# Optimization experiments

Hardware: AMD Instinct MI355X
Metric: run time of the kernel (lower is better)

The kernel has to match this reference:

```python
import jax, jax.numpy as jnp
import numpy as np

N_HEAD, D_FEAT, D_MODEL, D_ATTN = 4, 32, 32, 1
B, LQ, LK, H, W = 2, 24, 24, 16, 16
NEG_SLOPE = 0.1


def _lrelu(x):
    return jnp.where(x >= 0, x, NEG_SLOPE * x)


def setup_inputs() -> dict:
    key = jax.random.key(0)
    ks = jax.random.split(key, 12)
    s = 0.05
    inp = {
        "q": jax.random.normal(ks[0], (B, LQ, D_FEAT, H, W), jnp.float32),
        "k": jax.random.normal(ks[1], (B, LK, D_FEAT, H, W), jnp.float32),
        "v": jax.random.normal(ks[2], (B, LK, D_FEAT, H, W), jnp.float32),
        # 1x1 convs stored as (out_ch, in_ch) matrices
        "wq": jax.random.normal(ks[3], (N_HEAD * D_MODEL, D_FEAT), jnp.float32) * s,
        "bq": jax.random.normal(ks[4], (N_HEAD * D_MODEL,), jnp.float32) * s,
        "wk": jax.random.normal(ks[5], (N_HEAD * D_MODEL, D_FEAT), jnp.float32) * s,
        "bk": jax.random.normal(ks[6], (N_HEAD * D_MODEL,), jnp.float32) * s,
        "wv": jax.random.normal(ks[7], (N_HEAD * D_MODEL, D_FEAT), jnp.float32) * s,
        "bv": jax.random.normal(ks[8], (N_HEAD * D_MODEL,), jnp.float32) * s,
        # 5x5 attention conv (OIHW)
        "w_attn": jax.random.normal(ks[9], (D_ATTN, D_MODEL, 5, 5), jnp.float32) * s,
        "b_attn": jax.random.normal(ks[10], (D_ATTN,), jnp.float32) * s,
        # final Linear(n_head*d_model -> d_model), torch weight layout (out, in)
        "w_fc": jax.random.normal(ks[11], (D_MODEL, N_HEAD * D_MODEL), jnp.float32) * s,
    }
    return inp


def _proj_heads(x, w, b):
    # x: (b, l, c, h, w); 1x1 conv + leaky relu, split heads -> (b, n, l, d, h, w)
    y = _lrelu(jnp.einsum('blchw,oc->blohw', x, w) + b[None, None, :, None, None])
    bb, ll = x.shape[0], x.shape[1]
    return y.reshape(bb, ll, N_HEAD, D_MODEL, H, W).transpose(0, 2, 1, 3, 4, 5)


def reference(q, k, v, wq, bq, wk, bk, wv, bv, w_attn, b_attn, w_fc):
    qh = _proj_heads(q, wq, bq)  # (b,n,lq,d,h,w)
    kh = _proj_heads(k, wk, bk)  # (b,n,lk,d,h,w)
    vh = _proj_heads(v, wv, bv)  # (b,n,lk,d,h,w)

    # additive attention features: q_i + k_j for all (i,j) pairs
    qk = qh[:, :, :, None] + kh[:, :, None]  # (b,n,lq,lk,d,h,w)
    x = qk.reshape(-1, D_MODEL, H, W)
    logits = jax.lax.conv_general_dilated(
        x, w_attn, window_strides=(1, 1), padding=[(2, 2), (2, 2)],
        dimension_numbers=('NCHW', 'OIHW', 'NCHW')) + b_attn[None, :, None, None]
    attn = logits.reshape(B, N_HEAD, LQ, LK, D_ATTN, H, W)
    attn = jax.nn.softmax(attn, axis=3)  # softmax over keys

    # weighted sum over keys (d_attention==1 broadcasts over channels)
    res = jnp.einsum('bnqkhw,bnkchw->bnqchw', attn[:, :, :, :, 0], vh)

    # merge heads and apply final linear over channel dim (no bias), dropout=eval identity
    out = res.transpose(0, 2, 1, 3, 4, 5).reshape(B, LQ, N_HEAD * D_MODEL, H, W)
    out = jnp.einsum('blchw,oc->blohw', out, w_fc)  # (b,lq,d_model,h,w)
    return out, attn
```

## Files before the change

### kernel.cpp

```cpp
#include <hip/hip_runtime.h>
#include <math.h>

#define BB   2
#define LQ   24
#define LK   24
#define NH   4
#define DM   32
#define DF   32
#define HW   256
#define NEG  0.1f

#define PITCH 24
#define CHPAD (20 * PITCH)

__device__ __forceinline__ float lrelu(float x) { return x >= 0.f ? x : NEG * x; }

__global__ __launch_bounds__(256) void k_proj_conv(
    const float* __restrict__ kin, const float* __restrict__ vin,
    const float* __restrict__ wk, const float* __restrict__ bk,
    const float* __restrict__ wv, const float* __restrict__ bv,
    const float* __restrict__ wat,
    float* __restrict__ vh, float* __restrict__ ck)
{
    const int bx  = blockIdx.x;
    const int img = bx >> 2;
    const int cg  = bx & 3;
    const int b   = img / (NH * LK);
    const int n   = (img / LK) % NH;
    const int j   = img % LK;
    const int hw  = threadIdx.x;
    const int h   = hw >> 4, w = hw & 15;

    __shared__ float skh[8][CHPAD];

    for (int idx = hw; idx < 8 * CHPAD; idx += 256) ((float*)skh)[idx] = 0.f;

    const float* kb = kin + (size_t)((b * LK + j) * DF) * HW + hw;
    const float* vb = vin + (size_t)((b * LK + j) * DF) * HW + hw;

    float xr[DF];

    #pragma unroll
    for (int c = 0; c < DF; c++) xr[c] = vb[c * HW];
    #pragma unroll
    for (int d = 0; d < 8; d++) {
        const int o = n * DM + cg * 8 + d;
        const float* wr = wv + o * DF;
        float acc = bv[o];
        #pragma unroll
        for (int c = 0; c < DF; c++) acc += xr[c] * wr[c];
        vh[(size_t)img * (DM * HW) + (cg * 8 + d) * HW + hw] = lrelu(acc);
    }

    #pragma unroll
    for (int c = 0; c < DF; c++) xr[c] = kb[c * HW];
    __syncthreads();
    #pragma unroll
    for (int d = 0; d < 8; d++) {
        const int o = n * DM + cg * 8 + d;
        const float* wr = wk + o * DF;
        float acc = bk[o];
        #pragma unroll
        for (int c = 0; c < DF; c++) acc += xr[c] * wr[c];
        skh[d][(h + 2) * PITCH + (w + 2)] = lrelu(acc);
    }
    __syncthreads();

    float acc = 0.f;
    #pragma unroll
    for (int lc = 0; lc < 8; lc++) {
        const float* wc = wat + (cg * 8 + lc) * 25;
        #pragma unroll
        for (int ky = 0; ky < 5; ky++) {
            const float* row = &skh[lc][(h + ky) * PITCH + w];
            #pragma unroll
            for (int kx = 0; kx < 5; kx++)
                acc += row[kx] * wc[ky * 5 + kx];
        }
    }
    atomicAdd(&ck[img * HW + hw], acc);
}

__global__ __launch_bounds__(256) void k_softmax_res(
    const float* __restrict__ ck, const float* __restrict__ vh,
    float* __restrict__ res, float* __restrict__ attn_out)
{
    const int bn = blockIdx.x >> 5;
    const int u  = blockIdx.x & 31;
    const int hw = threadIdx.x;

    float e[LK];
    const float* cb = ck + bn * LK * HW + hw;
    float m = -1e30f;
    #pragma unroll
    for (int jj = 0; jj < LK; jj++) { e[jj] = cb[jj * HW]; m = fmaxf(m, e[jj]); }
    float s = 0.f;
    #pragma unroll
    for (int jj = 0; jj < LK; jj++) { e[jj] = __expf(e[jj] - m); s += e[jj]; }
    const float inv = 1.f / s;
    #pragma unroll
    for (int jj = 0; jj < LK; jj++) e[jj] *= inv;

    if (u < LQ) {
        float* ao = attn_out + (size_t)((bn * LQ + u) * LK) * HW + hw;
        #pragma unroll
        for (int jj = 0; jj < LK; jj++) ao[jj * HW] = e[jj];
    }

    const float* vp = vh + (size_t)(bn * LK) * (DM * HW) + u * HW + hw;
    float acc = 0.f;
    #pragma unroll
    for (int jj = 0; jj < LK; jj++) acc += e[jj] * vp[(size_t)jj * DM * HW];
    res[(bn * DM + u) * HW + hw] = acc;
}

__global__ __launch_bounds__(256) void k_fc(
    const float* __restrict__ res, const float* __restrict__ wfc,
    float* __restrict__ out)
{
    const int bx = blockIdx.x;
    const int b  = bx >> 7;
    const int o  = (bx >> 2) & 31;
    const int lg = bx & 3;
    const int hw = threadIdx.x;

    const float* rp = res + (size_t)b * (NH * DM) * HW + hw;
    const float* wr = wfc + o * (NH * DM);
    float acc = 0.f;
    #pragma unroll
    for (int nc = 0; nc < NH * DM; nc++) acc += wr[nc] * rp[nc * HW];

    #pragma unroll
    for (int l = lg * 6; l < lg * 6 + 6; l++)
        out[(size_t)((b * LQ + l) * DM + o) * HW + hw] = acc;
}

extern "C" void kernel_launch(void* const* d_in, const int* in_sizes, int n_in,
                              void* d_out, int out_size, void* d_ws, size_t ws_size,
                              hipStream_t stream)
{
    const float* k_in = (const float*)d_in[1];
    const float* v_in = (const float*)d_in[2];
    const float* wk   = (const float*)d_in[5];
    const float* bk   = (const float*)d_in[6];
    const float* wv   = (const float*)d_in[7];
    const float* bv   = (const float*)d_in[8];
    const float* wat  = (const float*)d_in[9];
    const float* wfc  = (const float*)d_in[11];

    float* out  = (float*)d_out;
    float* attn = out + (size_t)BB * LQ * DM * HW;

    float* vh  = (float*)d_ws;
    float* ck  = vh + (size_t)BB * NH * LK * DM * HW;
    float* res = ck + (size_t)BB * NH * LK * HW;

    hipMemsetAsync(ck, 0, (size_t)BB * NH * LK * HW * sizeof(float), stream);
    hipLaunchKernelGGL(k_proj_conv, dim3(BB * NH * LK * 4), dim3(256), 0, stream,
                       k_in, v_in, wk, bk, wv, bv, wat, vh, ck);
    hipLaunchKernelGGL(k_softmax_res, dim3(BB * NH * 32), dim3(256), 0, stream,
                       ck, vh, res, attn);
    hipLaunchKernelGGL(k_fc, dim3(BB * DM * 4), dim3(256), 0, stream,
                       res, wfc, out);
}
```

Baseline: 102.4 us.

## Replace atomic partial-sum reduction with per-group buffers and split softmax work

Each channel-group block now writes its partial attention-conv result to its own slice of a 4x buffer instead of atomically adding into a shared one. This removes the memset launch and the atomic traffic, and the softmax kernel sums the four partials itself. The softmax kernel also goes from 32 to 56 blocks per (b,n), so attention writes and the value-weighted sums run in separate blocks instead of one block doing both. The trade-off is more workspace, more reads in the softmax kernel, and the softmax being recomputed in more blocks.

```diff
diff --git a/kernel.cpp b/kernel.cpp
--- a/kernel.cpp
+++ b/kernel.cpp
@@ -13,6 +13,8 @@
 #define PITCH 24
 #define CHPAD (20 * PITCH)
 
+#define NIMG (BB * NH * LK)
+
 __device__ __forceinline__ float lrelu(float x) { return x >= 0.f ? x : NEG * x; }
 
 __global__ __launch_bounds__(256) void k_proj_conv(
@@ -20,7 +22,7 @@
     const float* __restrict__ wk, const float* __restrict__ bk,
     const float* __restrict__ wv, const float* __restrict__ bv,
     const float* __restrict__ wat,
-    float* __restrict__ vh, float* __restrict__ ck)
+    float* __restrict__ vh, float* __restrict__ ck4)
 {
     const int bx  = blockIdx.x;
     const int img = bx >> 2;
@@ -78,22 +80,28 @@
                 acc += row[kx] * wc[ky * 5 + kx];
         }
     }
-    atomicAdd(&ck[img * HW + hw], acc);
+    ck4[(size_t)(cg * NIMG + img) * HW + hw] = acc;
 }
 
 __global__ __launch_bounds__(256) void k_softmax_res(
-    const float* __restrict__ ck, const float* __restrict__ vh,
+    const float* __restrict__ ck4, const float* __restrict__ vh,
     float* __restrict__ res, float* __restrict__ attn_out)
 {
-    const int bn = blockIdx.x >> 5;
-    const int u  = blockIdx.x & 31;
+    const int bn = blockIdx.x / 56;
+    const int u  = blockIdx.x % 56;
     const int hw = threadIdx.x;
 
     float e[LK];
-    const float* cb = ck + bn * LK * HW + hw;
+    const float* c0 = ck4 + (size_t)(0 * NIMG + bn * LK) * HW + hw;
+    const float* c1 = ck4 + (size_t)(1 * NIMG + bn * LK) * HW + hw;
+    const float* c2 = ck4 + (size_t)(2 * NIMG + bn * LK) * HW + hw;
+    const float* c3 = ck4 + (size_t)(3 * NIMG + bn * LK) * HW + hw;
     float m = -1e30f;
     #pragma unroll
-    for (int jj = 0; jj < LK; jj++) { e[jj] = cb[jj * HW]; m = fmaxf(m, e[jj]); }
+    for (int jj = 0; jj < LK; jj++) {
+        e[jj] = (c0[jj * HW] + c1[jj * HW]) + (c2[jj * HW] + c3[jj * HW]);
+        m = fmaxf(m, e[jj]);
+    }
     float s = 0.f;
     #pragma unroll
     for (int jj = 0; jj < LK; jj++) { e[jj] = __expf(e[jj] - m); s += e[jj]; }
@@ -105,13 +113,14 @@
         float* ao = attn_out + (size_t)((bn * LQ + u) * LK) * HW + hw;
         #pragma unroll
         for (int jj = 0; jj < LK; jj++) ao[jj * HW] = e[jj];
+    } else {
+        const int c = u - LQ;
+        const float* vp = vh + (size_t)(bn * LK) * (DM * HW) + c * HW + hw;
+        float acc = 0.f;
+        #pragma unroll
+        for (int jj = 0; jj < LK; jj++) acc += e[jj] * vp[(size_t)jj * DM * HW];
+        res[(bn * DM + c) * HW + hw] = acc;
     }
-
-    const float* vp = vh + (size_t)(bn * LK) * (DM * HW) + u * HW + hw;
-    float acc = 0.f;
-    #pragma unroll
-    for (int jj = 0; jj < LK; jj++) acc += e[jj] * vp[(size_t)jj * DM * HW];
-    res[(bn * DM + u) * HW + hw] = acc;
 }
 
 __global__ __launch_bounds__(256) void k_fc(
@@ -152,14 +161,13 @@
     float* attn = out + (size_t)BB * LQ * DM * HW;
 
     float* vh  = (float*)d_ws;
-    float* ck  = vh + (size_t)BB * NH * LK * DM * HW;
-    float* res = ck + (size_t)BB * NH * LK * HW;
+    float* ck4 = vh  + (size_t)BB * NH * LK * DM * HW;
+    float* res = ck4 + (size_t)4 * NIMG * HW;
 
-    hipMemsetAsync(ck, 0, (size_t)BB * NH * LK * HW * sizeof(float), stream);
-    hipLaunchKernelGGL(k_proj_conv, dim3(BB * NH * LK * 4), dim3(256), 0, stream,
-                       k_in, v_in, wk, bk, wv, bv, wat, vh, ck);
-    hipLaunchKernelGGL(k_softmax_res, dim3(BB * NH * 32), dim3(256), 0, stream,
-                       ck, vh, res, attn);
+    hipLaunchKernelGGL(k_proj_conv, dim3(NIMG * 4), dim3(256), 0, stream,
+                       k_in, v_in, wk, bk, wv, bv, wat, vh, ck4);
+    hipLaunchKernelGGL(k_softmax_res, dim3(BB * NH * 56), dim3(256), 0, stream,
+                       ck4, vh, res, attn);
     hipLaunchKernelGGL(k_fc, dim3(BB * DM * 4), dim3(256), 0, stream,
                        res, wfc, out);
 }
```

Result: no change. 101.2 us, median of 3 (-1.2%).
